# Optimization experiments

Measured on AMD Instinct MI355X. Metric: run time of the kernel, lower is better.

The kernel has to match this reference:

```python
import jax, jax.numpy as jnp
import numpy as np

N_NODES = 50000
N_EDGES = 500000
HIDDEN = 128
N_LAYERS = 2


def setup_inputs() -> dict:
    key = jax.random.key(0)
    k1, k2, k3, k4, k5 = jax.random.split(key, 5)
    fea = jax.random.normal(k1, (N_NODES, HIDDEN), dtype=jnp.float32)
    adj_row = jax.random.randint(k2, (N_EDGES,), 0, N_NODES, dtype=jnp.int32)
    adj_col = jax.random.randint(k3, (N_EDGES,), 0, N_NODES, dtype=jnp.int32)
    adj_val = jax.random.uniform(k4, (N_EDGES,), dtype=jnp.float32)
    bias = jax.random.normal(k5, (N_LAYERS, HIDDEN), dtype=jnp.float32) * 0.088  # ~uniform(-stdv,stdv) scale
    return {"fea": fea, "adj_row": adj_row, "adj_col": adj_col, "adj_val": adj_val, "bias": bias}


def _spmm(x, row, col, val, n_nodes):
    # sparse [N,N] (COO) @ dense [N,d]: gather source rows, scale, scatter-add to dst
    msg = val[:, None] * x[col]                     # [E, d]
    return jax.ops.segment_sum(msg, row, num_segments=n_nodes)  # [N, d]


def reference(fea, adj_row, adj_col, adj_val, bias):
    n_nodes = fea.shape[0]
    n_layers = bias.shape[0]
    learn = fea
    tmp = fea
    for i in range(n_layers):
        # F.dropout is identity in eval mode
        learn = _spmm(learn, adj_row, adj_col, adj_val, n_nodes) + bias[i]
        tmp = tmp + learn
    return tmp / (n_layers + 1)
```

## Files before the change

kernel.cpp:

```cpp
#include <hip/hip_runtime.h>

#define HIDDEN 128
#define ELLW 32
#define GB   2048
#define TPB  256
#define NTH  (GB * TPB)
#define NWV  (NTH / 64)

typedef float v4f __attribute__((ext_vector_type(4)));

__device__ __forceinline__ unsigned f2bf(float f) {
    unsigned u = __float_as_uint(f);
    return (u + 0x7FFFu + ((u >> 16) & 1u)) >> 16;
}
__device__ __forceinline__ float bf2f(unsigned b) {
    return __uint_as_float(b << 16);
}


__global__ void build_kernel(const float* __restrict__ fea, unsigned short* __restrict__ fea16,
                             int n4, const int* __restrict__ row, const int* __restrict__ col,
                             const float* __restrict__ val, int* __restrict__ cnt,
                             unsigned* __restrict__ pairs, int E) {
    int g = blockIdx.x * TPB + threadIdx.x;
    for (int i = g; i < n4; i += NTH) {
        float4 v = ((const float4*)fea)[i];
        unsigned long long o =
              (unsigned long long)f2bf(v.x)
            | ((unsigned long long)f2bf(v.y) << 16)
            | ((unsigned long long)f2bf(v.z) << 32)
            | ((unsigned long long)f2bf(v.w) << 48);
        __builtin_nontemporal_store(o, (unsigned long long*)fea16 + i);
    }
    int E4 = E >> 2;
    for (int i = g; i < E4; i += NTH) {
        int4   r4 = ((const int4*)row)[i];
        int4   c4 = ((const int4*)col)[i];
        float4 v4 = ((const float4*)val)[i];
        int s0 = atomicAdd(&cnt[r4.x], 1);
        int s1 = atomicAdd(&cnt[r4.y], 1);
        int s2 = atomicAdd(&cnt[r4.z], 1);
        int s3 = atomicAdd(&cnt[r4.w], 1);
        if (s0 < ELLW) pairs[(size_t)r4.x * ELLW + s0] = (unsigned)c4.x | (f2bf(v4.x) << 16);
        if (s1 < ELLW) pairs[(size_t)r4.y * ELLW + s1] = (unsigned)c4.y | (f2bf(v4.y) << 16);
        if (s2 < ELLW) pairs[(size_t)r4.z * ELLW + s2] = (unsigned)c4.z | (f2bf(v4.z) << 16);
        if (s3 < ELLW) pairs[(size_t)r4.w * ELLW + s3] = (unsigned)c4.w | (f2bf(v4.w) << 16);
    }
    for (int e = (E4 << 2) + g; e < E; e += NTH) {
        int r = row[e];
        unsigned cv = (unsigned)col[e] | (f2bf(val[e]) << 16);
        int slot = atomicAdd(&cnt[r], 1);
        if (slot < ELLW) pairs[(size_t)r * ELLW + slot] = cv;
    }
}


__device__ __forceinline__ void gather_accum2(const unsigned short* __restrict__ src,
                                              unsigned myp, int mmax, int m, int lane, v4f& acc) {
    int q4 = (lane & 31) * 4;
    for (int j = 0; j < mmax; j += 16) {
        unsigned long long aa[16]; float vv[16];
        #pragma unroll
        for (int k = 0; k < 16; ++k) {
            int idx = j + k;
            unsigned pe = __shfl(myp, idx, 32);
            bool ok = idx < m;
            vv[k] = ok ? bf2f(pe >> 16) : 0.0f;
            aa[k] = *(const unsigned long long*)(src + (size_t)(ok ? (pe & 0xFFFFu) : 0u) * HIDDEN + q4);
        }
        #pragma unroll
        for (int k = 0; k < 16; ++k) {
            acc.x += vv[k] * bf2f((unsigned)aa[k] & 0xFFFFu);
            acc.y += vv[k] * bf2f(((unsigned)aa[k] >> 16));
            acc.z += vv[k] * bf2f((unsigned)(aa[k] >> 32) & 0xFFFFu);
            acc.w += vv[k] * bf2f((unsigned)(aa[k] >> 48));
        }
    }
}

__global__ void gather1_kernel(const unsigned short* __restrict__ x16,
                               const int* __restrict__ cnt,
                               const unsigned* __restrict__ pairs,
                               const float* __restrict__ bias0,
                               unsigned short* __restrict__ y16, int n) {
    int lane = threadIdx.x & 63;
    int wv = (blockIdx.x * TPB + threadIdx.x) >> 6;
    int q = lane & 31;
    v4f b0 = *(const v4f*)(bias0 + q * 4);
    int nw = (n + 1) >> 1;
    for (int w = wv; w < nw; w += NWV) {
        int node = 2 * w + (lane >> 5);
        bool valid = node < n;
        int nn = valid ? node : (n - 1);
        unsigned myp = pairs[(size_t)nn * ELLW + q];
        int m = valid ? cnt[nn] : 0; if (m > ELLW) m = ELLW;
        int mmax = max(m, __shfl_xor(m, 32, 64));
        v4f acc = b0;
        gather_accum2(x16, myp, mmax, m, lane, acc);
        unsigned long long o =
              (unsigned long long)f2bf(acc.x)
            | ((unsigned long long)f2bf(acc.y) << 16)
            | ((unsigned long long)f2bf(acc.z) << 32)
            | ((unsigned long long)f2bf(acc.w) << 48);
        if (valid)
            __builtin_nontemporal_store(o,
                (unsigned long long*)(y16 + (size_t)nn * HIDDEN + q * 4));
    }
}

__global__ void gather2_kernel(const unsigned short* __restrict__ l16,
                               const unsigned short* __restrict__ fea16,
                               const int* __restrict__ cnt,
                               const unsigned* __restrict__ pairs,
                               const float* __restrict__ bias1,
                               float* __restrict__ out, int n) {
    int lane = threadIdx.x & 63;
    int wv = (blockIdx.x * TPB + threadIdx.x) >> 6;
    int q = lane & 31;
    v4f bb = *(const v4f*)(bias1 + q * 4);
    const float s = 1.0f / 3.0f;
    int nw = (n + 1) >> 1;
    for (int w = wv; w < nw; w += NWV) {
        int node = 2 * w + (lane >> 5);
        bool valid = node < n;
        int nn = valid ? node : (n - 1);
        size_t b = (size_t)nn * HIDDEN + q * 4;
        unsigned myp = __builtin_nontemporal_load(&pairs[(size_t)nn * ELLW + q]);
        int m = valid ? cnt[nn] : 0; if (m > ELLW) m = ELLW;
        int mmax = max(m, __shfl_xor(m, 32, 64));
        unsigned long long fw   = *(const unsigned long long*)(fea16 + b);
        unsigned long long lown = *(const unsigned long long*)(l16 + b);
        v4f acc;
        acc.x = bf2f((unsigned)fw & 0xFFFFu)         + bf2f((unsigned)lown & 0xFFFFu)         + bb.x;
        acc.y = bf2f((unsigned)fw >> 16)             + bf2f((unsigned)lown >> 16)             + bb.y;
        acc.z = bf2f((unsigned)(fw >> 32) & 0xFFFFu) + bf2f((unsigned)(lown >> 32) & 0xFFFFu) + bb.z;
        acc.w = bf2f((unsigned)(fw >> 48))           + bf2f((unsigned)(lown >> 48))           + bb.w;
        gather_accum2(l16, myp, mmax, m, lane, acc);
        v4f r = acc * s;
        if (valid)
            __builtin_nontemporal_store(r, (v4f*)(out + b));
    }
}


__global__ void scatter_kernel(const float* __restrict__ x, const int* __restrict__ row,
                               const int* __restrict__ col, const float* __restrict__ val,
                               float* __restrict__ out, int n_edges, float scale) {
    long long gid = (long long)blockIdx.x * blockDim.x + threadIdx.x;
    int e = (int)(gid >> 6);
    int lane = (int)(gid & 63);
    if (e >= n_edges) return;
    float v = val[e] * scale;
    float2 p = ((const float2*)(x + (size_t)col[e] * HIDDEN))[lane];
    float* o = out + (size_t)row[e] * HIDDEN + 2 * lane;
    atomicAdd(o, v * p.x);
    atomicAdd(o + 1, v * p.y);
}

__global__ void add_bias_kernel(float* __restrict__ buf, const float* __restrict__ bias, int n4) {
    int i = blockIdx.x * blockDim.x + threadIdx.x;
    if (i >= n4) return;
    float4 x = ((float4*)buf)[i];
    float4 bb = ((const float4*)bias)[i & 31];
    x.x += bb.x; x.y += bb.y; x.z += bb.z; x.w += bb.w;
    ((float4*)buf)[i] = x;
}

__global__ void out_init_kernel(const float* __restrict__ fea, const float* __restrict__ learn1,
                                const float* __restrict__ bias1, float* __restrict__ out, int n4) {
    int i = blockIdx.x * blockDim.x + threadIdx.x;
    if (i >= n4) return;
    float4 a = ((const float4*)fea)[i];
    float4 b = ((const float4*)learn1)[i];
    float4 c = ((const float4*)bias1)[i & 31];
    const float s = 1.0f / 3.0f;
    ((float4*)out)[i] = make_float4((a.x + b.x + c.x) * s, (a.y + b.y + c.y) * s,
                                    (a.z + b.z + c.z) * s, (a.w + b.w + c.w) * s);
}

extern "C" void kernel_launch(void* const* d_in, const int* in_sizes, int n_in,
                              void* d_out, int out_size, void* d_ws, size_t ws_size,
                              hipStream_t stream) {
    const float* fea  = (const float*)d_in[0];
    const int*   row  = (const int*)d_in[1];
    const int*   col  = (const int*)d_in[2];
    const float* val  = (const float*)d_in[3];
    const float* bias = (const float*)d_in[4];
    float* out = (float*)d_out;

    const int N = in_sizes[0] / HIDDEN;
    const int E = in_sizes[1];

    size_t off = 0;
    auto alloc = [&](size_t bytes) {
        void* p = (char*)d_ws + off;
        off = (off + bytes + 255) & ~(size_t)255;
        return p;
    };
    int*      cnt   = (int*)alloc((size_t)N * sizeof(int));
    unsigned* pairs = (unsigned*)alloc((size_t)N * ELLW * sizeof(unsigned));
    unsigned short* fea16   = (unsigned short*)alloc((size_t)N * HIDDEN * sizeof(short));
    unsigned short* learn16 = (unsigned short*)alloc((size_t)N * HIDDEN * sizeof(short));
    size_t off_full = off;

    const int n4 = N * HIDDEN / 4;

    if (off_full <= ws_size && N <= 65535) {
        (void)hipMemsetAsync(cnt, 0, (size_t)N * sizeof(int), stream);
        build_kernel<<<GB, TPB, 0, stream>>>(fea, fea16, n4, row, col, val, cnt, pairs, E);
        gather1_kernel<<<GB, TPB, 0, stream>>>(fea16, cnt, pairs, bias, learn16, N);
        gather2_kernel<<<GB, TPB, 0, stream>>>(learn16, fea16, cnt, pairs, bias + HIDDEN, out, N);
    } else {
        float* learn1 = (float*)d_ws;
        (void)hipMemsetAsync(learn1, 0, (size_t)N * HIDDEN * sizeof(float), stream);
        long long sc_threads = (long long)E * 64;
        int sc_blocks = (int)((sc_threads + 255) / 256);
        scatter_kernel<<<sc_blocks, 256, 0, stream>>>(fea, row, col, val, learn1, E, 1.0f);
        int ewb = (n4 + 255) / 256;
        add_bias_kernel<<<ewb, 256, 0, stream>>>(learn1, bias, n4);
        out_init_kernel<<<ewb, 256, 0, stream>>>(fea, learn1, bias + HIDDEN, out, n4);
        scatter_kernel<<<sc_blocks, 256, 0, stream>>>(learn1, row, col, val, out, E, 1.0f / 3.0f);
    }
}
```

Baseline: 157.6 us.

## Partition ELL build edges by destination row range per XCD block group

The edge-to-ELL build now has groups of 8 blocks scan the same edge chunk, and each block handles only destinations in its eighth of the row range. With round-robin block dispatch, this is meant to keep each row's counter atomics and slot writes on one XCD's L2, avoiding cross-die coherence traffic. In exchange the row array is read eight times and the vectorized int4 edge loads are replaced with scalar loads.

```diff
diff --git a/kernel.cpp b/kernel.cpp
--- a/kernel.cpp
+++ b/kernel.cpp
@@ -21,8 +21,9 @@
 __global__ void build_kernel(const float* __restrict__ fea, unsigned short* __restrict__ fea16,
                              int n4, const int* __restrict__ row, const int* __restrict__ col,
                              const float* __restrict__ val, int* __restrict__ cnt,
-                             unsigned* __restrict__ pairs, int E) {
-    int g = blockIdx.x * TPB + threadIdx.x;
+                             unsigned* __restrict__ pairs, int E, int chunk, int RPX) {
+    int tid = threadIdx.x;
+    int g = blockIdx.x * TPB + tid;
     for (int i = g; i < n4; i += NTH) {
         float4 v = ((const float4*)fea)[i];
         unsigned long long o =
@@ -32,25 +33,18 @@
             | ((unsigned long long)f2bf(v.w) << 48);
         __builtin_nontemporal_store(o, (unsigned long long*)fea16 + i);
     }
-    int E4 = E >> 2;
-    for (int i = g; i < E4; i += NTH) {
-        int4   r4 = ((const int4*)row)[i];
-        int4   c4 = ((const int4*)col)[i];
-        float4 v4 = ((const float4*)val)[i];
-        int s0 = atomicAdd(&cnt[r4.x], 1);
-        int s1 = atomicAdd(&cnt[r4.y], 1);
-        int s2 = atomicAdd(&cnt[r4.z], 1);
-        int s3 = atomicAdd(&cnt[r4.w], 1);
-        if (s0 < ELLW) pairs[(size_t)r4.x * ELLW + s0] = (unsigned)c4.x | (f2bf(v4.x) << 16);
-        if (s1 < ELLW) pairs[(size_t)r4.y * ELLW + s1] = (unsigned)c4.y | (f2bf(v4.y) << 16);
-        if (s2 < ELLW) pairs[(size_t)r4.z * ELLW + s2] = (unsigned)c4.z | (f2bf(v4.z) << 16);
-        if (s3 < ELLW) pairs[(size_t)r4.w * ELLW + s3] = (unsigned)c4.w | (f2bf(v4.w) << 16);
-    }
-    for (int e = (E4 << 2) + g; e < E; e += NTH) {
+    int grp = blockIdx.x >> 3;
+    unsigned lbl_lo = (unsigned)((blockIdx.x & 7) * RPX);
+    int lo = grp * chunk;
+    int hi = lo + chunk; if (hi > E) hi = E;
+    for (int e = lo + tid; e < hi; e += TPB) {
         int r = row[e];
-        unsigned cv = (unsigned)col[e] | (f2bf(val[e]) << 16);
-        int slot = atomicAdd(&cnt[r], 1);
-        if (slot < ELLW) pairs[(size_t)r * ELLW + slot] = cv;
+        if ((unsigned)r - lbl_lo < (unsigned)RPX) {
+            unsigned cv = (unsigned)col[e] | (f2bf(val[e]) << 16);
+            int slot = atomicAdd(&cnt[r], 1);
+            if (slot < ELLW)
+                pairs[(size_t)r * ELLW + slot] = cv;
+        }
     }
 }
 
@@ -204,10 +198,14 @@
     size_t off_full = off;
 
     const int n4 = N * HIDDEN / 4;
+    const int NG = GB / 8;
+    const int chunk = (E + NG - 1) / NG;
+    const int RPX = (N + 7) / 8;
 
     if (off_full <= ws_size && N <= 65535) {
         (void)hipMemsetAsync(cnt, 0, (size_t)N * sizeof(int), stream);
-        build_kernel<<<GB, TPB, 0, stream>>>(fea, fea16, n4, row, col, val, cnt, pairs, E);
+        build_kernel<<<GB, TPB, 0, stream>>>(fea, fea16, n4, row, col, val,
+                                             cnt, pairs, E, chunk, RPX);
         gather1_kernel<<<GB, TPB, 0, stream>>>(fea16, cnt, pairs, bias, learn16, N);
         gather2_kernel<<<GB, TPB, 0, stream>>>(learn16, fea16, cnt, pairs, bias + HIDDEN, out, N);
     } else {
```

Result: no change. 156.1 us (-0.9%).
